# Kernel optimization log

Hardware: AMD Instinct MI355X
Metric: run time of the kernel (lower is better)

## Reference

```python
import jax, jax.numpy as jnp
import numpy as np

T, B, D, H = 32, 128, 256, 768
MAX_PONDER = 8
EPS = 0.01


def setup_inputs() -> dict:
    key = jax.random.key(0)
    ks = jax.random.split(key, 6)
    s = 1.0 / np.sqrt(H)
    return {
        "input_": jax.random.normal(ks[0], (T, B, D), jnp.float32),
        "W_ih": jax.random.uniform(ks[1], (H, D + 1), jnp.float32, -s, s),
        "W_hh": jax.random.uniform(ks[2], (H, H), jnp.float32, -s, s),
        "b_ih": jax.random.uniform(ks[3], (H,), jnp.float32, -s, s),
        "b_hh": jax.random.uniform(ks[4], (H,), jnp.float32, -s, s),
        "w_p": jax.random.uniform(ks[5], (H,), jnp.float32, -s, s),
        "b_p": jnp.ones((1,), jnp.float32),  # torch reset_parameters fills ponder bias with 1
    }


def reference(input_, W_ih, W_hh, b_ih, b_hh, w_p, b_p):
    T_, B_, D_ = input_.shape
    H_ = W_hh.shape[0]
    dt = input_.dtype
    hx0 = jnp.zeros((B_, H_), dt)

    def time_step(carry, x_t):
        hx, pcost = carry

        def ponder(c, _):
            hx_i, ah, ahx, sc, spc, mask, flag = c
            # input row with ponder flag (0 on first act step, 1 afterwards)
            x_in = jnp.concatenate([x_t, jnp.full((B_, 1), flag, dt)], axis=1)
            # ponder cost assigned for active rows before update
            spc = jnp.where(mask, -ah, spc)
            hx_new = jnp.tanh(x_in @ W_ih.T + b_ih + hx_i @ W_hh.T + b_hh)
            hx_i = jnp.where(mask[:, None], hx_new, hx_i)
            mf = mask.astype(dt)
            ahx = ahx + mf[:, None] * hx_new  # accum_hx += hx (as in source)
            h = jax.nn.sigmoid(hx_new @ w_p + b_p[0])
            ah2 = ah + mf * h
            p = h - jnp.maximum(ah2 - 1.0, 0.0)
            ahx = ahx + (mf * p)[:, None] * hx_new  # accum_hx += p*hx
            sc = sc + mf
            mask2 = ah2 < (1.0 - EPS)
            return (hx_i, ah2, ahx, sc, spc, mask2, jnp.ones((), dt)), None

        init = (hx,
                jnp.zeros((B_,), dt),           # accum_h
                jnp.zeros((B_, H_), dt),        # accum_hx
                jnp.zeros((B_,), dt),           # step_count
                jnp.zeros((B_,), dt),           # step_ponder_cost
                jnp.ones((B_,), bool),          # selector
                jnp.zeros((), dt))              # flag
        (hx_i, ah, ahx, sc, spc, mask, flag), _ = jax.lax.scan(
            ponder, init, None, length=MAX_PONDER)
        hx_out = ahx / sc[:, None]
        return (hx_out, pcost + spc), (hx_out, sc)

    (hx_last, pcost), (all_hx, steps) = jax.lax.scan(
        time_step, (hx0, jnp.zeros((B_,), dt)), input_)
    # all_hx: [T,B,H], hx: [1,B,H], ponder_cost: [B], ponder_times: [T,B]
    return all_hx, hx_last[None], pcost, steps
```

## Files before the change

kernel.cpp:

```cpp
#include <hip/hip_runtime.h>
#include <math.h>

#define TT 32
#define BB 128
#define DD 256
#define HH 768
#define MAXP 8

#define RG   8
#define RPG  16
#define CB   12
#define CS   64
#define NTH  256
#define NCH  24

#define OFF_LAST  ((size_t)TT * BB * HH)
#define OFF_PCOST (OFF_LAST + (size_t)BB * HH)
#define OFF_STEPS (OFF_PCOST + BB)

#define ASCOPE __HIP_MEMORY_SCOPE_AGENT

typedef __attribute__((ext_vector_type(8))) short s16x8;
typedef __attribute__((ext_vector_type(4))) float f32x4;
typedef unsigned long long ull;

static __device__ __forceinline__ unsigned short f2bf(float f) {
    unsigned u = __float_as_uint(f);
    u = (u + 0x7fffu + ((u >> 16) & 1u)) >> 16;
    return (unsigned short)u;
}
static __device__ __forceinline__ float bf2f(unsigned short h) {
    return __uint_as_float(((unsigned)h) << 16);
}
static __device__ __forceinline__ float fast_tanh(float v) {
    return 1.f - 2.f / (__expf(2.f * v) + 1.f);
}

__launch_bounds__(NTH, 1)
__global__ void act_kernel(const float* __restrict__ x,
                           const float* __restrict__ Wih,
                           const float* __restrict__ Whh,
                           const float* __restrict__ bih,
                           const float* __restrict__ bhh,
                           const float* __restrict__ wpv,
                           const float* __restrict__ bp,
                           float* __restrict__ out,
                           unsigned* __restrict__ flags,
                           s16x8* __restrict__ hxe,
                           float* __restrict__ zpt)
{
    const int tid  = threadIdx.x;
    const int rg   = blockIdx.x & 7;
    const int cbk  = blockIdx.x >> 3;
    const int r0   = rg * RPG;
    const int c0   = cbk * CS;
    const int CT   = tid >> 6;
    const int lane = tid & 63;
    const int am   = lane & 15;
    const int aq   = lane >> 4;

    __shared__ s16x8 A_s[NCH * 64];
    __shared__ s16x8 WB_s[4 * 8 * 64];
    __shared__ s16x8 xA_s[8 * 64];
    __shared__ unsigned short hxn_s[RPG][72];
    __shared__ float wp_s[CS];

    s16x8 Breg[NCH];
    {
        const float* wr = Whh + (size_t)(c0 + CT*16 + am) * HH + aq*8;
        for (int ch = 0; ch < NCH; ++ch) {
            float4 a0 = *(const float4*)(wr + ch*32);
            float4 a1 = *(const float4*)(wr + ch*32 + 4);
            union { s16x8 v; unsigned short e[8]; } u;
            u.e[0]=f2bf(a0.x); u.e[1]=f2bf(a0.y); u.e[2]=f2bf(a0.z); u.e[3]=f2bf(a0.w);
            u.e[4]=f2bf(a1.x); u.e[5]=f2bf(a1.y); u.e[6]=f2bf(a1.z); u.e[7]=f2bf(a1.w);
            Breg[ch] = u.v;
        }
    }
    for (int ch = 0; ch < 8; ++ch) {
        const float* wr = Wih + (size_t)(c0 + CT*16 + am) * (DD+1) + ch*32 + aq*8;
        union { s16x8 v; unsigned short e[8]; } u;
        #pragma unroll
        for (int j = 0; j < 8; ++j) u.e[j] = f2bf(wr[j]);
        WB_s[(CT*8 + ch)*64 + lane] = u.v;
    }
    if (tid < CS) wp_s[tid] = wpv[c0 + tid];
    const int myc = c0 + CT*16 + am;
    const float bs_lane = bih[myc] + bhh[myc];
    const float wfl     = Wih[(size_t)myc*(DD+1) + DD];
    const float bp0     = bp[0];
    {
        s16x8 z8 = {0,0,0,0,0,0,0,0};
        #pragma unroll
        for (int j = 0; j < 6; ++j) A_s[j*NTH + tid] = z8;
    }

    float pc = 0.f;
    unsigned it = 0;

    auto publish = [&]() {
        const unsigned par = it & 1u;
        if (CT == 0) {
            ull*   exw = (ull*)(hxe + (size_t)(rg*2 + par) * (NCH*64));
            float* zpw = zpt + (size_t)(rg*2 + par) * (RPG*CB);
            const ull* s0 = (const ull*)&hxn_s[am][aq*8];
            const ull* s1 = (const ull*)&hxn_s[am][32 + aq*8];
            ull* d0 = exw + ((size_t)(2*cbk)*64   + lane)*2;
            ull* d1 = exw + ((size_t)(2*cbk+1)*64 + lane)*2;
            __hip_atomic_store(d0,   s0[0], __ATOMIC_RELAXED, ASCOPE);
            __hip_atomic_store(d0+1, s0[1], __ATOMIC_RELAXED, ASCOPE);
            __hip_atomic_store(d1,   s1[0], __ATOMIC_RELAXED, ASCOPE);
            __hip_atomic_store(d1+1, s1[1], __ATOMIC_RELAXED, ASCOPE);
            const int zr = lane >> 2, zc = lane & 3;
            float sz = 0.f;
            #pragma unroll
            for (int i = 0; i < 16; ++i)
                sz += bf2f(hxn_s[zr][zc*16 + i]) * wp_s[zc*16 + i];
            sz += __shfl_xor(sz, 1);
            sz += __shfl_xor(sz, 2);
            if (zc == 0)
                __hip_atomic_store(&zpw[zr*CB + cbk], sz, __ATOMIC_RELAXED, ASCOPE);
            asm volatile("s_waitcnt vmcnt(0)" ::: "memory");
            if (lane == 0)
                __hip_atomic_store(&flags[rg*16 + cbk], it + 1u, __ATOMIC_RELAXED, ASCOPE);
        }
        ++it;
    };

    for (int t = 0; t < TT; ++t) {
        #pragma unroll
        for (int j = 0; j < 2; ++j) {
            const int s = j*NTH + tid;
            const int ch = s >> 6;
            const float* xb = x + ((size_t)t*BB + r0 + am)*DD + ch*32 + aq*8;
            float4 a0 = *(const float4*)xb;
            float4 a1 = *(const float4*)(xb + 4);
            union { s16x8 v; unsigned short e[8]; } u;
            u.e[0]=f2bf(a0.x); u.e[1]=f2bf(a0.y); u.e[2]=f2bf(a0.z); u.e[3]=f2bf(a0.w);
            u.e[4]=f2bf(a1.x); u.e[5]=f2bf(a1.y); u.e[6]=f2bf(a1.z); u.e[7]=f2bf(a1.w);
            xA_s[s] = u.v;
        }
        __syncthreads();

        f32x4 xi;
        {
            f32x4 a = {0.f,0.f,0.f,0.f};
            #pragma unroll
            for (int ch = 0; ch < 8; ++ch)
                a = __builtin_amdgcn_mfma_f32_16x16x32_bf16(
                        xA_s[ch*64 + lane], WB_s[(CT*8 + ch)*64 + lane], a, 0, 0, 0);
            xi[0]=a[0]+bs_lane; xi[1]=a[1]+bs_lane; xi[2]=a[2]+bs_lane; xi[3]=a[3]+bs_lane;
        }

        float ahx[48];
        #pragma unroll
        for (int q = 0; q < 48; ++q) ahx[q] = 0.f;
        float ah = 0.f, sc = 0.f, spc = 0.f;
        int act = 1;

        {
            f32x4 acc = xi;
            #pragma unroll
            for (int ch = 0; ch < NCH; ++ch)
                acc = __builtin_amdgcn_mfma_f32_16x16x32_bf16(
                        A_s[ch*64 + lane], Breg[ch], acc, 0, 0, 0);
            #pragma unroll
            for (int r = 0; r < 4; ++r)
                hxn_s[aq*4 + r][CT*16 + am] = f2bf(fast_tanh(acc[r]));
        }
        __syncthreads();
        publish();

        for (int pk = 1; ; ++pk) {
            if (CT == 0) {
                const int pi = lane % 12;
                unsigned v;
                do { v = __hip_atomic_load(&flags[rg*16 + pi], __ATOMIC_RELAXED, ASCOPE); }
                while (!__all((int)(v >= it)));
            }
            __syncthreads();

            const unsigned parR = (it - 1u) & 1u;
            const ull*   exr = (const ull*)(hxe + (size_t)(rg*2 + parR) * (NCH*64));
            const float* zpr = zpt + (size_t)(rg*2 + parR) * (RPG*CB);

            ull clo[6], chi[6];
            #pragma unroll
            for (int j = 0; j < 6; ++j) {
                const ull* src = exr + ((size_t)((j*4 + CT)*64 + lane))*2;
                clo[j] = __hip_atomic_load(src,     __ATOMIC_RELAXED, ASCOPE);
                chi[j] = __hip_atomic_load(src + 1, __ATOMIC_RELAXED, ASCOPE);
            }
            ull zu[6];
            {
                const ull* zb = (const ull*)(zpr + am*CB);
                #pragma unroll
                for (int j = 0; j < 6; ++j)
                    zu[j] = __hip_atomic_load(zb + j, __ATOMIC_RELAXED, ASCOPE);
            }
            #pragma unroll
            for (int j = 0; j < 6; ++j) {
                union { ull u[2]; s16x8 v; } cv;
                cv.u[0] = clo[j]; cv.u[1] = chi[j];
                A_s[(j*4 + CT)*64 + lane] = cv.v;
            }

            float zf[12];
            #pragma unroll
            for (int j = 0; j < 6; ++j) {
                zf[2*j]   = __uint_as_float((unsigned)(zu[j] & 0xffffffffu));
                zf[2*j+1] = __uint_as_float((unsigned)(zu[j] >> 32));
            }
            const float zA = (zf[0]+zf[1]) + (zf[2]+zf[3]);
            const float zB = (zf[4]+zf[5]) + (zf[6]+zf[7]);
            const float zC = (zf[8]+zf[9]) + (zf[10]+zf[11]);
            const float z  = (zA + zB) + zC;
            const float h  = 1.f / (1.f + __expf(-(z + bp0)));
            float w1 = 0.f;
            if (act) {
                spc = -ah;
                ah += h;
                w1 = 1.f + (h - fmaxf(ah - 1.f, 0.f));
                sc += 1.f;
                act = (ah < 0.99f) ? 1 : 0;
            }
            const bool done = __all(act == 0) || (pk == MAXP);

            if (done) {
                #pragma unroll
                for (int j = 0; j < 6; ++j) {
                    #pragma unroll
                    for (int i = 0; i < 4; ++i) {
                        ahx[j*8 + i]     += w1 * bf2f((unsigned short)(clo[j] >> (16*i)));
                        ahx[j*8 + 4 + i] += w1 * bf2f((unsigned short)(chi[j] >> (16*i)));
                    }
                }
                break;
            }
            __syncthreads();

            f32x4 acc = xi;
            #pragma unroll
            for (int ch = 0; ch < NCH; ++ch)
                acc = __builtin_amdgcn_mfma_f32_16x16x32_bf16(
                        A_s[ch*64 + lane], Breg[ch], acc, 0, 0, 0);
            #pragma unroll
            for (int j = 0; j < 6; ++j) {
                #pragma unroll
                for (int i = 0; i < 4; ++i) {
                    ahx[j*8 + i]     += w1 * bf2f((unsigned short)(clo[j] >> (16*i)));
                    ahx[j*8 + 4 + i] += w1 * bf2f((unsigned short)(chi[j] >> (16*i)));
                }
            }
            #pragma unroll
            for (int r = 0; r < 4; ++r)
                hxn_s[aq*4 + r][CT*16 + am] = f2bf(fast_tanh(acc[r] + wfl));
            __syncthreads();
            publish();
        }

        const float inv = 1.f / sc;
        pc += spc;
        if (cbk == 0 && tid < RPG) out[OFF_STEPS + (size_t)t*BB + r0 + tid] = sc;
        #pragma unroll
        for (int j = 0; j < 6; ++j) {
            const int ch = j*4 + CT;
            float o[8];
            #pragma unroll
            for (int i = 0; i < 8; ++i) o[i] = ahx[j*8 + i] * inv;
            union { s16x8 v; unsigned short e[8]; } u;
            #pragma unroll
            for (int i = 0; i < 8; ++i) u.e[i] = f2bf(o[i]);
            A_s[ch*64 + lane] = u.v;
            if (cbk == 0) {
                float* op = out + ((size_t)t*BB + r0 + am)*HH + ch*32 + aq*8;
                *(float4*)op       = make_float4(o[0], o[1], o[2], o[3]);
                *(float4*)(op + 4) = make_float4(o[4], o[5], o[6], o[7]);
                if (t == TT-1) {
                    float* lp = out + OFF_LAST + (size_t)(r0 + am)*HH + ch*32 + aq*8;
                    *(float4*)lp       = make_float4(o[0], o[1], o[2], o[3]);
                    *(float4*)(lp + 4) = make_float4(o[4], o[5], o[6], o[7]);
                }
            }
        }
    }
    if (cbk == 0 && tid < RPG) out[OFF_PCOST + r0 + tid] = pc;
}

extern "C" void kernel_launch(void* const* d_in, const int* in_sizes, int n_in,
                              void* d_out, int out_size, void* d_ws, size_t ws_size,
                              hipStream_t stream) {
    const float* x   = (const float*)d_in[0];
    const float* Wih = (const float*)d_in[1];
    const float* Whh = (const float*)d_in[2];
    const float* bih = (const float*)d_in[3];
    const float* bhh = (const float*)d_in[4];
    const float* wpv = (const float*)d_in[5];
    const float* bp  = (const float*)d_in[6];
    float* out = (float*)d_out;

    unsigned* flags = (unsigned*)d_ws;
    s16x8*    hxe   = (s16x8*)((char*)d_ws + 4096);
    float*    zpt   = (float*)((char*)d_ws + 4096 + (size_t)RG*2*NCH*64*16);

    hipMemsetAsync(d_ws, 0, 4096, stream);
    act_kernel<<<dim3(RG*CB), dim3(NTH), 0, stream>>>(
        x, Wih, Whh, bih, bhh, wpv, bp, out, flags, hxe, zpt);
}
```

Before: 352.4 us.

## Replace flag-based inter-block sync with sentinel-valued data polling and 4-deep buffers

Removes the per-block flag counter and its vmcnt wait. Consumers now poll the exchanged hidden-state and ponder partial-sum words directly until none hold an all-ones sentinel, then re-arm a buffer two slots ahead by writing the sentinel back. The buffer ring grows from 2 to 4 slots, and all 256 threads take part in publishing instead of one wavefront. This cuts a serial flag round trip from each ponder step. The cost is more polling loads, and correctness now rests on relaxed-store visibility per word and on no real value matching the sentinel bit pattern.

```diff
diff --git a/kernel.cpp b/kernel.cpp
--- a/kernel.cpp
+++ b/kernel.cpp
@@ -13,12 +13,14 @@
 #define CS   64
 #define NTH  256
 #define NCH  24
+#define NBUF 4
 
 #define OFF_LAST  ((size_t)TT * BB * HH)
 #define OFF_PCOST (OFF_LAST + (size_t)BB * HH)
 #define OFF_STEPS (OFF_PCOST + BB)
 
 #define ASCOPE __HIP_MEMORY_SCOPE_AGENT
+#define SENT   0xFFFFFFFFFFFFFFFFull
 
 typedef __attribute__((ext_vector_type(8))) short s16x8;
 typedef __attribute__((ext_vector_type(4))) float f32x4;
@@ -45,8 +47,7 @@
                            const float* __restrict__ wpv,
                            const float* __restrict__ bp,
                            float* __restrict__ out,
-                           unsigned* __restrict__ flags,
-                           s16x8* __restrict__ hxe,
+                           ull* __restrict__ hxe,
                            float* __restrict__ zpt)
 {
     const int tid  = threadIdx.x;
@@ -59,10 +60,17 @@
     const int am   = lane & 15;
     const int aq   = lane >> 4;
 
+    const int pchd  = tid >> 7;
+    const int pl    = (tid & 127) >> 1;
+    const int phalf = tid & 1;
+    const int prow  = pl & 15;
+    const int pcol  = pchd*32 + (pl >> 4)*8 + phalf*4;
+    const size_t pword = ((size_t)(2*cbk + pchd)*64 + pl)*2 + phalf;
+
     __shared__ s16x8 A_s[NCH * 64];
     __shared__ s16x8 WB_s[4 * 8 * 64];
     __shared__ s16x8 xA_s[8 * 64];
-    __shared__ unsigned short hxn_s[RPG][72];
+    __shared__ __align__(16) unsigned short hxn_s[RPG][72];
     __shared__ float wp_s[CS];
 
     s16x8 Breg[NCH];
@@ -99,18 +107,12 @@
     unsigned it = 0;
 
     auto publish = [&]() {
-        const unsigned par = it & 1u;
+        const unsigned par = it & (NBUF-1);
+        ull*   exw = hxe + (size_t)(rg*NBUF + par) * (NCH*64*2);
+        float* zpw = zpt + (size_t)(rg*NBUF + par) * (RPG*CB);
+        __hip_atomic_store(exw + pword, *(const ull*)&hxn_s[prow][pcol],
+                           __ATOMIC_RELAXED, ASCOPE);
         if (CT == 0) {
-            ull*   exw = (ull*)(hxe + (size_t)(rg*2 + par) * (NCH*64));
-            float* zpw = zpt + (size_t)(rg*2 + par) * (RPG*CB);
-            const ull* s0 = (const ull*)&hxn_s[am][aq*8];
-            const ull* s1 = (const ull*)&hxn_s[am][32 + aq*8];
-            ull* d0 = exw + ((size_t)(2*cbk)*64   + lane)*2;
-            ull* d1 = exw + ((size_t)(2*cbk+1)*64 + lane)*2;
-            __hip_atomic_store(d0,   s0[0], __ATOMIC_RELAXED, ASCOPE);
-            __hip_atomic_store(d0+1, s0[1], __ATOMIC_RELAXED, ASCOPE);
-            __hip_atomic_store(d1,   s1[0], __ATOMIC_RELAXED, ASCOPE);
-            __hip_atomic_store(d1+1, s1[1], __ATOMIC_RELAXED, ASCOPE);
             const int zr = lane >> 2, zc = lane & 3;
             float sz = 0.f;
             #pragma unroll
@@ -120,9 +122,6 @@
             sz += __shfl_xor(sz, 2);
             if (zc == 0)
                 __hip_atomic_store(&zpw[zr*CB + cbk], sz, __ATOMIC_RELAXED, ASCOPE);
-            asm volatile("s_waitcnt vmcnt(0)" ::: "memory");
-            if (lane == 0)
-                __hip_atomic_store(&flags[rg*16 + cbk], it + 1u, __ATOMIC_RELAXED, ASCOPE);
         }
         ++it;
     };
@@ -172,44 +171,60 @@
         publish();
 
         for (int pk = 1; ; ++pk) {
-            if (CT == 0) {
-                const int pi = lane % 12;
-                unsigned v;
-                do { v = __hip_atomic_load(&flags[rg*16 + pi], __ATOMIC_RELAXED, ASCOPE); }
-                while (!__all((int)(v >= it)));
-            }
-            __syncthreads();
-
-            const unsigned parR = (it - 1u) & 1u;
-            const ull*   exr = (const ull*)(hxe + (size_t)(rg*2 + parR) * (NCH*64));
-            const float* zpr = zpt + (size_t)(rg*2 + parR) * (RPG*CB);
-
-            ull clo[6], chi[6];
-            #pragma unroll
-            for (int j = 0; j < 6; ++j) {
-                const ull* src = exr + ((size_t)((j*4 + CT)*64 + lane))*2;
-                clo[j] = __hip_atomic_load(src,     __ATOMIC_RELAXED, ASCOPE);
-                chi[j] = __hip_atomic_load(src + 1, __ATOMIC_RELAXED, ASCOPE);
-            }
-            ull zu[6];
+            const unsigned rpar = (it - 1u) & (NBUF-1);
+            const ull* exr = hxe + (size_t)(rg*NBUF + rpar) * (NCH*64*2);
+            const ull* zbr = (const ull*)(zpt + (size_t)(rg*NBUF + rpar) * (RPG*CB) + am*CB);
+
+            ull hv[12], zv[6];
+            unsigned hok = 0, zok = 0;
+            for (;;) {
+                #pragma unroll
+                for (int j = 0; j < 6; ++j) {
+                    const ull* src = exr + ((size_t)((j*4 + CT)*64 + lane))*2;
+                    if (!(hok & (1u << (2*j)))) {
+                        hv[2*j] = __hip_atomic_load(src, __ATOMIC_RELAXED, ASCOPE);
+                        if (hv[2*j] != SENT) hok |= 1u << (2*j);
+                    }
+                    if (!(hok & (1u << (2*j+1)))) {
+                        hv[2*j+1] = __hip_atomic_load(src+1, __ATOMIC_RELAXED, ASCOPE);
+                        if (hv[2*j+1] != SENT) hok |= 1u << (2*j+1);
+                    }
+                }
+                #pragma unroll
+                for (int j = 0; j < 6; ++j) {
+                    if (!(zok & (1u << j))) {
+                        zv[j] = __hip_atomic_load(zbr + j, __ATOMIC_RELAXED, ASCOPE);
+                        if ((unsigned)(zv[j] & 0xffffffffu) != 0xffffffffu &&
+                            (unsigned)(zv[j] >> 32)         != 0xffffffffu)
+                            zok |= 1u << j;
+                    }
+                }
+                if (__all((int)(hok == 0xfffu && zok == 0x3fu))) break;
+            }
+
             {
-                const ull* zb = (const ull*)(zpr + am*CB);
-                #pragma unroll
-                for (int j = 0; j < 6; ++j)
-                    zu[j] = __hip_atomic_load(zb + j, __ATOMIC_RELAXED, ASCOPE);
-            }
+                const unsigned cpar = (it + 1u) & (NBUF-1);
+                ull*   exc = hxe + (size_t)(rg*NBUF + cpar) * (NCH*64*2);
+                float* zpc = zpt + (size_t)(rg*NBUF + cpar) * (RPG*CB);
+                __hip_atomic_store(exc + pword, SENT, __ATOMIC_RELAXED, ASCOPE);
+                if (tid < RPG)
+                    __hip_atomic_store(&zpc[tid*CB + cbk],
+                                       __uint_as_float(0xffffffffu),
+                                       __ATOMIC_RELAXED, ASCOPE);
+            }
+
             #pragma unroll
             for (int j = 0; j < 6; ++j) {
                 union { ull u[2]; s16x8 v; } cv;
-                cv.u[0] = clo[j]; cv.u[1] = chi[j];
+                cv.u[0] = hv[2*j]; cv.u[1] = hv[2*j+1];
                 A_s[(j*4 + CT)*64 + lane] = cv.v;
             }
 
             float zf[12];
             #pragma unroll
             for (int j = 0; j < 6; ++j) {
-                zf[2*j]   = __uint_as_float((unsigned)(zu[j] & 0xffffffffu));
-                zf[2*j+1] = __uint_as_float((unsigned)(zu[j] >> 32));
+                zf[2*j]   = __uint_as_float((unsigned)(zv[j] & 0xffffffffu));
+                zf[2*j+1] = __uint_as_float((unsigned)(zv[j] >> 32));
             }
             const float zA = (zf[0]+zf[1]) + (zf[2]+zf[3]);
             const float zB = (zf[4]+zf[5]) + (zf[6]+zf[7]);
@@ -231,8 +246,8 @@
                 for (int j = 0; j < 6; ++j) {
                     #pragma unroll
                     for (int i = 0; i < 4; ++i) {
-                        ahx[j*8 + i]     += w1 * bf2f((unsigned short)(clo[j] >> (16*i)));
-                        ahx[j*8 + 4 + i] += w1 * bf2f((unsigned short)(chi[j] >> (16*i)));
+                        ahx[j*8 + i]     += w1 * bf2f((unsigned short)(hv[2*j]   >> (16*i)));
+                        ahx[j*8 + 4 + i] += w1 * bf2f((unsigned short)(hv[2*j+1] >> (16*i)));
                     }
                 }
                 break;
@@ -248,8 +263,8 @@
             for (int j = 0; j < 6; ++j) {
                 #pragma unroll
                 for (int i = 0; i < 4; ++i) {
-                    ahx[j*8 + i]     += w1 * bf2f((unsigned short)(clo[j] >> (16*i)));
-                    ahx[j*8 + 4 + i] += w1 * bf2f((unsigned short)(chi[j] >> (16*i)));
+                    ahx[j*8 + i]     += w1 * bf2f((unsigned short)(hv[2*j]   >> (16*i)));
+                    ahx[j*8 + 4 + i] += w1 * bf2f((unsigned short)(hv[2*j+1] >> (16*i)));
                 }
             }
             #pragma unroll
@@ -299,11 +314,11 @@
     const float* bp  = (const float*)d_in[6];
     float* out = (float*)d_out;
 
-    unsigned* flags = (unsigned*)d_ws;
-    s16x8*    hxe   = (s16x8*)((char*)d_ws + 4096);
-    float*    zpt   = (float*)((char*)d_ws + 4096 + (size_t)RG*2*NCH*64*16);
-
-    hipMemsetAsync(d_ws, 0, 4096, stream);
+    ull*   hxe = (ull*)d_ws;
+    float* zpt = (float*)((char*)d_ws + (size_t)RG*NBUF*NCH*64*16);
+
+    hipMemsetAsync(d_ws, 0xFF, (size_t)RG*NBUF*NCH*64*16 + (size_t)RG*NBUF*RPG*CB*4,
+                   stream);
     act_kernel<<<dim3(RG*CB), dim3(NTH), 0, stream>>>(
-        x, Wih, Whh, bih, bhh, wpv, bp, out, flags, hxe, zpt);
-}
+        x, Wih, Whh, bih, bhh, wpv, bp, out, hxe, zpt);
+}
```

New measurement: 437.0 us. 24.0% more time.

## Consume per-producer exchange chunks as flags arrive instead of waiting for all

Applied to the files above, without the earlier changes.

The wait loop in wave 0 now polls producer flags and immediately loads each ready producer's hidden-state chunk and partial ponder sums into shared memory, rather than waiting for all twelve and then having every wave load. The ponder-sum reduction and the accumulation read through shared memory, and one block barrier per ponder step is removed. This is meant to overlap exchange latency with flag polling, at the cost of serialising all global loads onto a single wave.

```diff
diff --git a/kernel.cpp b/kernel.cpp
--- a/kernel.cpp
+++ b/kernel.cpp
@@ -35,6 +35,8 @@
 static __device__ __forceinline__ float fast_tanh(float v) {
     return 1.f - 2.f / (__expf(2.f * v) + 1.f);
 }
+
+union AU { f32x4 f; s16x8 s; unsigned short e[8]; ull u[2]; };
 
 __launch_bounds__(NTH, 1)
 __global__ void act_kernel(const float* __restrict__ x,
@@ -46,7 +48,7 @@
                            const float* __restrict__ bp,
                            float* __restrict__ out,
                            unsigned* __restrict__ flags,
-                           s16x8* __restrict__ hxe,
+                           ull* __restrict__ hxe,
                            float* __restrict__ zpt)
 {
     const int tid  = threadIdx.x;
@@ -62,7 +64,8 @@
     __shared__ s16x8 A_s[NCH * 64];
     __shared__ s16x8 WB_s[4 * 8 * 64];
     __shared__ s16x8 xA_s[8 * 64];
-    __shared__ unsigned short hxn_s[RPG][72];
+    __shared__ __align__(16) unsigned short hxn_s[RPG][72];
+    __shared__ float zred_s[RPG][CB];
     __shared__ float wp_s[CS];
 
     s16x8 Breg[NCH];
@@ -101,16 +104,18 @@
     auto publish = [&]() {
         const unsigned par = it & 1u;
         if (CT == 0) {
-            ull*   exw = (ull*)(hxe + (size_t)(rg*2 + par) * (NCH*64));
+            ull*   exw = hxe + (size_t)(rg*2 + par) * (NCH*64*2);
             float* zpw = zpt + (size_t)(rg*2 + par) * (RPG*CB);
-            const ull* s0 = (const ull*)&hxn_s[am][aq*8];
-            const ull* s1 = (const ull*)&hxn_s[am][32 + aq*8];
+            const ull s00 = ((const ull*)&hxn_s[am][aq*8])[0];
+            const ull s01 = ((const ull*)&hxn_s[am][aq*8])[1];
+            const ull s10 = ((const ull*)&hxn_s[am][32 + aq*8])[0];
+            const ull s11 = ((const ull*)&hxn_s[am][32 + aq*8])[1];
             ull* d0 = exw + ((size_t)(2*cbk)*64   + lane)*2;
             ull* d1 = exw + ((size_t)(2*cbk+1)*64 + lane)*2;
-            __hip_atomic_store(d0,   s0[0], __ATOMIC_RELAXED, ASCOPE);
-            __hip_atomic_store(d0+1, s0[1], __ATOMIC_RELAXED, ASCOPE);
-            __hip_atomic_store(d1,   s1[0], __ATOMIC_RELAXED, ASCOPE);
-            __hip_atomic_store(d1+1, s1[1], __ATOMIC_RELAXED, ASCOPE);
+            __hip_atomic_store(d0,   s00, __ATOMIC_RELAXED, ASCOPE);
+            __hip_atomic_store(d0+1, s01, __ATOMIC_RELAXED, ASCOPE);
+            __hip_atomic_store(d1,   s10, __ATOMIC_RELAXED, ASCOPE);
+            __hip_atomic_store(d1+1, s11, __ATOMIC_RELAXED, ASCOPE);
             const int zr = lane >> 2, zc = lane & 3;
             float sz = 0.f;
             #pragma unroll
@@ -173,44 +178,43 @@
 
         for (int pk = 1; ; ++pk) {
             if (CT == 0) {
+                const unsigned parR = (it - 1u) & 1u;
+                const ull*   exr = hxe + (size_t)(rg*2 + parR) * (NCH*64*2);
+                const float* zpr = zpt + (size_t)(rg*2 + parR) * (RPG*CB);
                 const int pi = lane % 12;
-                unsigned v;
-                do { v = __hip_atomic_load(&flags[rg*16 + pi], __ATOMIC_RELAXED, ASCOPE); }
-                while (!__all((int)(v >= it)));
+                unsigned done_m = 0;
+                while (done_m != 0xfffu) {
+                    const unsigned v =
+                        __hip_atomic_load(&flags[rg*16 + pi], __ATOMIC_RELAXED, ASCOPE);
+                    ull rdy = __ballot((lane < 12) && (v >= it) &&
+                                       !((done_m >> lane) & 1u));
+                    while (rdy) {
+                        const int p = (int)__builtin_ctzll(rdy);
+                        rdy &= rdy - 1;
+                        done_m |= 1u << p;
+                        const ull* s0 = exr + ((size_t)(2*p)*64   + lane)*2;
+                        const ull* s1 = exr + ((size_t)(2*p+1)*64 + lane)*2;
+                        AU c0, c1;
+                        c0.u[0] = __hip_atomic_load(s0,   __ATOMIC_RELAXED, ASCOPE);
+                        c0.u[1] = __hip_atomic_load(s0+1, __ATOMIC_RELAXED, ASCOPE);
+                        c1.u[0] = __hip_atomic_load(s1,   __ATOMIC_RELAXED, ASCOPE);
+                        c1.u[1] = __hip_atomic_load(s1+1, __ATOMIC_RELAXED, ASCOPE);
+                        float zl = 0.f;
+                        if (lane < RPG)
+                            zl = __uint_as_float(__hip_atomic_load(
+                                     (const unsigned*)&zpr[lane*CB + p],
+                                     __ATOMIC_RELAXED, ASCOPE));
+                        A_s[(2*p)*64   + lane] = c0.s;
+                        A_s[(2*p+1)*64 + lane] = c1.s;
+                        if (lane < RPG) zred_s[lane][p] = zl;
+                    }
+                }
             }
             __syncthreads();
 
-            const unsigned parR = (it - 1u) & 1u;
-            const ull*   exr = (const ull*)(hxe + (size_t)(rg*2 + parR) * (NCH*64));
-            const float* zpr = zpt + (size_t)(rg*2 + parR) * (RPG*CB);
-
-            ull clo[6], chi[6];
-            #pragma unroll
-            for (int j = 0; j < 6; ++j) {
-                const ull* src = exr + ((size_t)((j*4 + CT)*64 + lane))*2;
-                clo[j] = __hip_atomic_load(src,     __ATOMIC_RELAXED, ASCOPE);
-                chi[j] = __hip_atomic_load(src + 1, __ATOMIC_RELAXED, ASCOPE);
-            }
-            ull zu[6];
-            {
-                const ull* zb = (const ull*)(zpr + am*CB);
-                #pragma unroll
-                for (int j = 0; j < 6; ++j)
-                    zu[j] = __hip_atomic_load(zb + j, __ATOMIC_RELAXED, ASCOPE);
-            }
-            #pragma unroll
-            for (int j = 0; j < 6; ++j) {
-                union { ull u[2]; s16x8 v; } cv;
-                cv.u[0] = clo[j]; cv.u[1] = chi[j];
-                A_s[(j*4 + CT)*64 + lane] = cv.v;
-            }
-
             float zf[12];
             #pragma unroll
-            for (int j = 0; j < 6; ++j) {
-                zf[2*j]   = __uint_as_float((unsigned)(zu[j] & 0xffffffffu));
-                zf[2*j+1] = __uint_as_float((unsigned)(zu[j] >> 32));
-            }
+            for (int k = 0; k < 12; ++k) zf[k] = zred_s[am][k];
             const float zA = (zf[0]+zf[1]) + (zf[2]+zf[3]);
             const float zB = (zf[4]+zf[5]) + (zf[6]+zf[7]);
             const float zC = (zf[8]+zf[9]) + (zf[10]+zf[11]);
@@ -229,15 +233,13 @@
             if (done) {
                 #pragma unroll
                 for (int j = 0; j < 6; ++j) {
+                    AU u; u.s = A_s[(j*4 + CT)*64 + lane];
                     #pragma unroll
-                    for (int i = 0; i < 4; ++i) {
-                        ahx[j*8 + i]     += w1 * bf2f((unsigned short)(clo[j] >> (16*i)));
-                        ahx[j*8 + 4 + i] += w1 * bf2f((unsigned short)(chi[j] >> (16*i)));
-                    }
+                    for (int i = 0; i < 8; ++i)
+                        ahx[j*8 + i] += w1 * bf2f(u.e[i]);
                 }
                 break;
             }
-            __syncthreads();
 
             f32x4 acc = xi;
             #pragma unroll
@@ -246,11 +248,10 @@
                         A_s[ch*64 + lane], Breg[ch], acc, 0, 0, 0);
             #pragma unroll
             for (int j = 0; j < 6; ++j) {
+                AU u; u.s = A_s[(j*4 + CT)*64 + lane];
                 #pragma unroll
-                for (int i = 0; i < 4; ++i) {
-                    ahx[j*8 + i]     += w1 * bf2f((unsigned short)(clo[j] >> (16*i)));
-                    ahx[j*8 + 4 + i] += w1 * bf2f((unsigned short)(chi[j] >> (16*i)));
-                }
+                for (int i = 0; i < 8; ++i)
+                    ahx[j*8 + i] += w1 * bf2f(u.e[i]);
             }
             #pragma unroll
             for (int r = 0; r < 4; ++r)
@@ -300,7 +301,7 @@
     float* out = (float*)d_out;
 
     unsigned* flags = (unsigned*)d_ws;
-    s16x8*    hxe   = (s16x8*)((char*)d_ws + 4096);
+    ull*      hxe   = (ull*)((char*)d_ws + 4096);
     float*    zpt   = (float*)((char*)d_ws + 4096 + (size_t)RG*2*NCH*64*16);
 
     hipMemsetAsync(d_ws, 0, 4096, stream);
```

Result: slower. 571.1 us (+62.1%).
